# Kernel tuning notes

Hardware: AMD Instinct MI355X
Metric: run time of the kernel (lower is better)

Reference implementation:

```python
import jax, jax.numpy as jnp
import numpy as np

B, IN_DIM, C, H, W = 4, 64, 128, 64, 64
HW = H * W
EPS = 1e-5


def _conv(x, w, b, pad):
    y = jax.lax.conv_general_dilated(
        x, w, (1, 1), [(pad, pad), (pad, pad)],
        dimension_numbers=('NCHW', 'OIHW', 'NCHW'))
    return y + b[None, :, None, None]


def _ln_chw(x, g, b):
    # torch LayerNorm([C,H,W]): normalize over (C,H,W) per sample, affine per-element
    m = jnp.mean(x, axis=(1, 2, 3), keepdims=True)
    v = jnp.mean((x - m) ** 2, axis=(1, 2, 3), keepdims=True)
    return (x - m) * jax.lax.rsqrt(v + EPS) * g[None] + b[None]


def _lrelu(x):
    return jnp.where(x >= 0, x, 0.01 * x)


def setup_inputs():
    ks = jax.random.split(jax.random.key(0), 16)

    def n(i, shape, s):
        return jax.random.normal(ks[i], shape, jnp.float32) * s

    inp = {
        'f_e': n(0, (B, IN_DIM, H, W), 1.0),
        'f_i': n(1, (B, IN_DIM, H, W), 1.0),
        'w1': n(2, (C, IN_DIM, 3, 3), 0.04), 'b1': jnp.zeros((C,), jnp.float32),
        'g1': jnp.ones((C, H, W), jnp.float32), 'be1': jnp.zeros((C, H, W), jnp.float32),
        'w2': n(3, (C, IN_DIM, 3, 3), 0.04), 'b2': jnp.zeros((C,), jnp.float32),
        'g2': jnp.ones((C, H, W), jnp.float32), 'be2': jnp.zeros((C, H, W), jnp.float32),
        'W3': n(4, (HW, HW), 0.015), 'b3': jnp.zeros((HW,), jnp.float32),
        'W4': n(5, (C, C), 0.08), 'b4': jnp.zeros((C,), jnp.float32),
        'W5': n(6, (C, C), 0.08), 'b5': jnp.zeros((C,), jnp.float32),
        'w6a': n(7, (C, C, 1, 1), 0.08), 'b6a': jnp.zeros((C,), jnp.float32),
        'g6a': jnp.ones((C, H, W), jnp.float32), 'be6a': jnp.zeros((C, H, W), jnp.float32),
        'w6b': n(8, (C, C, 3, 3), 0.03), 'b6b': jnp.zeros((C,), jnp.float32),
        'g6b': jnp.ones((C, H, W), jnp.float32), 'be6b': jnp.zeros((C, H, W), jnp.float32),
        'wf': n(9, (IN_DIM, C, 1, 1), 0.08), 'bf': jnp.zeros((IN_DIM,), jnp.float32),
    }
    return inp


def reference(f_e, f_i, w1, b1, g1, be1, w2, b2, g2, be2, W3, b3, W4, b4,
              W5, b5, w6a, b6a, g6a, be6a, w6b, b6b, g6b, be6b, wf, bf):
    b_, _, h, w = f_e.shape
    c = w1.shape[0]
    hw = h * w

    # f_1: conv3x3 -> LN([C,H,W]) -> LeakyReLU -> b (hw) c
    x1 = _lrelu(_ln_chw(_conv(f_e, w1, b1, 1), g1, be1))
    f_e_1 = x1.transpose(0, 2, 3, 1).reshape(b_, hw, c)

    # f_2: conv3x3 -> LN -> LeakyReLU (stays b c h w)
    f_i_2 = _lrelu(_ln_chw(_conv(f_i, w2, b2, 1), g2, be2))

    # f_3: b c (hw) -> Linear(HW,HW) -> LeakyReLU
    f_i_3 = _lrelu(jnp.einsum('bcn,mn->bcm', f_i_2.reshape(b_, c, hw), W3) + b3)

    # f_4: b (hw) c -> Linear(C,C) -> LeakyReLU
    tok = f_i_2.transpose(0, 2, 3, 1).reshape(b_, hw, c)
    f_e_4 = _lrelu(jnp.einsum('bnc,dc->bnd', tok, W4) + b4)

    # unscaled single-head attention over hw tokens
    scores = jnp.einsum('bnc,bcm->bnm', f_e_4, f_i_3)   # (b, hw, hw)
    attn = jax.nn.softmax(scores, axis=-1)
    f_e_5_in = jnp.einsum('bnm,bmc->bnc', attn, f_e_1)

    # f_5: Linear(C,C) -> LeakyReLU -> b c h w
    f_e_5 = _lrelu(jnp.einsum('bnc,dc->bnd', f_e_5_in, W5) + b5)
    f_e_5 = f_e_5.reshape(b_, h, w, c).transpose(0, 3, 1, 2)

    # f_6: conv1x1 -> LN -> LReLU -> conv3x3 -> LN -> LReLU
    y = _lrelu(_ln_chw(_conv(f_i_2, w6a, b6a, 0), g6a, be6a))
    f_i_6 = _lrelu(_ln_chw(_conv(y, w6b, b6b, 1), g6b, be6b))

    f_e_7 = f_e_5 * f_i_6
    f_e_8 = _conv(f_e_7, wf, bf, 0)
    return (f_e_8, f_i_2)
```

## Files before the change

### kernel.cpp

```cpp
#include <hip/hip_runtime.h>

typedef unsigned short ushort_t;
typedef unsigned int uint_t;
typedef unsigned long long u64_t;

#define Bn 4
#define IND 64
#define Cn 128
#define Nn 4096
#define CN 524288
#define BUF 2097152

typedef __attribute__((ext_vector_type(8))) __bf16 bf16x8;
typedef __attribute__((ext_vector_type(4))) float f32x4;

__device__ __forceinline__ float b2f(ushort_t s) {
    return __uint_as_float(((uint_t)s) << 16);
}
__device__ __forceinline__ ushort_t f2b(float f) {
    uint_t u = __float_as_uint(f);
    uint_t r = u + 0x7fffu + ((u >> 16) & 1u);
    return (ushort_t)(r >> 16);
}
__device__ __forceinline__ void unpack8(uint4 u, float* f) {
    f[0] = __uint_as_float(u.x << 16); f[1] = __uint_as_float(u.x & 0xffff0000u);
    f[2] = __uint_as_float(u.y << 16); f[3] = __uint_as_float(u.y & 0xffff0000u);
    f[4] = __uint_as_float(u.z << 16); f[5] = __uint_as_float(u.z & 0xffff0000u);
    f[6] = __uint_as_float(u.w << 16); f[7] = __uint_as_float(u.w & 0xffff0000u);
}
__device__ __forceinline__ float lrelu(float x) { return x >= 0.f ? x : 0.01f * x; }

__device__ __forceinline__ float getv(const float* p, size_t i) { return p[i]; }
__device__ __forceinline__ float getv(const ushort_t* p, size_t i) { return b2f(p[i]); }
__device__ __forceinline__ float4 get4(const float* p, size_t i) { return *(const float4*)(p + i); }
__device__ __forceinline__ float4 get4(const ushort_t* p, size_t i) {
    ushort4 u = *(const ushort4*)(p + i);
    float4 f = {b2f(u.x), b2f(u.y), b2f(u.z), b2f(u.w)};
    return f;
}
__device__ __forceinline__ void stv(float* p, float v) { *p = v; }
__device__ __forceinline__ void stv(ushort_t* p, float v) { *p = f2b(v); }

__device__ __forceinline__ uint4 pack8(float4 a, float4 b) {
    uint4 r;
    r.x = (uint_t)f2b(a.x) | ((uint_t)f2b(a.y) << 16);
    r.y = (uint_t)f2b(a.z) | ((uint_t)f2b(a.w) << 16);
    r.z = (uint_t)f2b(b.x) | ((uint_t)f2b(b.y) << 16);
    r.w = (uint_t)f2b(b.z) | ((uint_t)f2b(b.w) << 16);
    return r;
}

__global__ void detect_kernel(const void* g1, int* flag) {
    if (threadIdx.x == 0 && blockIdx.x == 0)
        *flag = (((const ushort_t*)g1)[0] == 0x3F80) ? 0 : 1;
}

template <int CI>
__global__ __launch_bounds__(256) void wtrans(const void* w, ushort_t* Wt, const int* flagp) {
    int F = *flagp;
    int idx = blockIdx.x * 256 + threadIdx.x;
    if (idx >= 128 * 9 * CI) return;
    int co = idx / (9 * CI);
    int rem = idx - co * 9 * CI;
    int tap = rem / CI;
    int ci = rem - tap * CI;
    size_t srci = (size_t)co * CI * 9 + (size_t)ci * 9 + tap;
    float v = F ? ((const float*)w)[srci] : b2f(((const ushort_t*)w)[srci]);
    Wt[idx] = f2b(v);
}

template <typename TEXT>
__device__ __forceinline__ void tin_body(const TEXT* src, ushort_t* dst, float (*tile)[33]) {
    int b = blockIdx.z, c0 = blockIdx.y * 32, n0 = blockIdx.x * 32;
    int nx = threadIdx.x & 31, cy = threadIdx.x >> 5;
    #pragma unroll
    for (int s = 0; s < 4; s++) {
        int cl = cy + s * 8;
        tile[cl][nx] = getv(src, ((size_t)(b * 64 + c0 + cl)) * 4096 + n0 + nx);
    }
    __syncthreads();
    #pragma unroll
    for (int s = 0; s < 4; s++) {
        int nl = cy + s * 8;
        dst[((size_t)b * 4096 + n0 + nl) * 64 + c0 + nx] = f2b(tile[nx][nl]);
    }
}

__global__ __launch_bounds__(256) void transpose_in(const void* src, ushort_t* dst, const int* flagp) {
    __shared__ float tile[32][33];
    int F = *flagp;
    if (F) tin_body((const float*)src, dst, tile);
    else   tin_body((const ushort_t*)src, dst, tile);
}

template <int CI>
__global__ __launch_bounds__(512, 2) void conv_mfma(const ushort_t* __restrict__ Xt,
                                                    const ushort_t* __restrict__ Wt,
                                                    const void* bias, float* __restrict__ out,
                                                    const int* flagp) {
    constexpr int RS = CI + 8;
    constexpr int SROWS = 195;
    constexpr int SBYTES = SROWS * RS * 2;
    constexpr int OBYTES = 128 * 68 * 4;
    constexpr int SMEM = SBYTES > OBYTES ? SBYTES : OBYTES;
    __shared__ __align__(16) char smem[SMEM];
    ushort_t* S = (ushort_t*)smem;
    float* Ob = (float*)smem;

    int t = threadIdx.x;
    int blk = blockIdx.x;
    int b = blk >> 6, y = blk & 63;
    int n0 = y << 6;

    constexpr int RQ = CI / 8;
    constexpr int CNT = SROWS * RQ;
    for (int i = t; i < CNT; i += 512) {
        int s = i / RQ;
        int c8 = (i - s * RQ) * 8;
        int tok = n0 + s - 65;
        uint4 v = {0u, 0u, 0u, 0u};
        if (s < 194 && (unsigned)tok < 4096u)
            v = *(const uint4*)(Xt + ((size_t)b * 4096 + tok) * CI + c8);
        *(uint4*)(S + (size_t)s * RS + c8) = v;
    }
    __syncthreads();

    int lane = t & 63, w = t >> 6;
    int li = lane & 15, q = lane >> 4;
    int px0 = 16 * (w & 3);
    int coh = 64 * (w >> 2);
    int x = px0 + li;

    f32x4 acc[4];
    #pragma unroll
    for (int T = 0; T < 4; T++) acc[T] = {0.f, 0.f, 0.f, 0.f};

    #pragma unroll
    for (int tap = 0; tap < 9; tap++) {
        int dy = tap / 3 - 1, dx = tap % 3 - 1;
        bool vx = (unsigned)(x + dx) < 64u;
        int srow = x + dy * 64 + dx + 65;
        int sr2 = vx ? srow : 194;
        #pragma unroll
        for (int ks = 0; ks < CI / 32; ks++) {
            bf16x8 a = *(const bf16x8*)(S + (size_t)sr2 * RS + ks * 32 + q * 8);
            #pragma unroll
            for (int T = 0; T < 4; T++) {
                int co = coh + 16 * T + li;
                bf16x8 bb = *(const bf16x8*)(Wt + ((size_t)co * 9 + tap) * CI + ks * 32 + q * 8);
                acc[T] = __builtin_amdgcn_mfma_f32_16x16x32_bf16(a, bb, acc[T], 0, 0, 0);
            }
        }
    }
    __syncthreads();

    int F = *flagp;
    #pragma unroll
    for (int T = 0; T < 4; T++) {
        int co = coh + 16 * T + li;
        float bv = F ? ((const float*)bias)[co] : b2f(((const ushort_t*)bias)[co]);
        #pragma unroll
        for (int rr = 0; rr < 4; rr++)
            Ob[(size_t)co * 68 + px0 + 4 * q + rr] = acc[T][rr] + bv;
    }
    __syncthreads();
    for (int i = t; i < 2048; i += 512) {
        int co = i >> 4, p4 = (i & 15) * 4;
        *(uint4*)(out + ((size_t)(b * 128 + co)) * 4096 + n0 + p4) =
            *(const uint4*)(Ob + (size_t)co * 68 + p4);
    }
}

__global__ __launch_bounds__(256) void ln_reduce1(const float* __restrict__ src,
                                                  float* __restrict__ part) {
    int t = threadIdx.x;
    size_t base = (size_t)blockIdx.x * 1024 + t * 4;
    float4 v = *(const float4*)(src + base);
    float s = v.x + v.y + v.z + v.w;
    float q = v.x * v.x + v.y * v.y + v.z * v.z + v.w * v.w;
    for (int off = 32; off > 0; off >>= 1) {
        s += __shfl_down(s, off, 64);
        q += __shfl_down(q, off, 64);
    }
    __shared__ float red[8];
    if ((t & 63) == 0) { red[(t >> 6) * 2] = s; red[(t >> 6) * 2 + 1] = q; }
    __syncthreads();
    if (t == 0) {
        s = red[0] + red[2] + red[4] + red[6];
        q = red[1] + red[3] + red[5] + red[7];
        part[blockIdx.x * 2] = s;
        part[blockIdx.x * 2 + 1] = q;
    }
}

__global__ __launch_bounds__(256) void ln_reduce2(const float* __restrict__ part,
                                                  float* __restrict__ der) {
    int b = blockIdx.x, t = threadIdx.x;
    float s = part[(b * 512 + t) * 2] + part[(b * 512 + 256 + t) * 2];
    float q = part[(b * 512 + t) * 2 + 1] + part[(b * 512 + 256 + t) * 2 + 1];
    for (int off = 32; off > 0; off >>= 1) {
        s += __shfl_down(s, off, 64);
        q += __shfl_down(q, off, 64);
    }
    __shared__ float red[8];
    if ((t & 63) == 0) { red[(t >> 6) * 2] = s; red[(t >> 6) * 2 + 1] = q; }
    __syncthreads();
    if (t == 0) {
        s = red[0] + red[2] + red[4] + red[6];
        q = red[1] + red[3] + red[5] + red[7];
        float mean = s * (1.f / (float)CN);
        float var = q * (1.f / (float)CN) - mean * mean;
        der[b * 2] = mean;
        der[b * 2 + 1] = rsqrtf(var + 1e-5f);
    }
}

template <typename TEXT, typename TOD, int HT, int HD>
__device__ __forceinline__ void ln_body(const float* src, const TEXT* g, const TEXT* be,
                                        const float* der, ushort_t* outT, TOD* outD,
                                        float (*tile)[33]) {
    int b = blockIdx.z, c0 = blockIdx.y * 32, n0 = blockIdx.x * 32;
    float mean = der[b * 2], rstd = der[b * 2 + 1];
    int nx = threadIdx.x & 31, cy = threadIdx.x >> 5;
    #pragma unroll
    for (int s = 0; s < 4; s++) {
        int cl = cy + s * 8;
        int c = c0 + cl;
        size_t gi = (size_t)c * Nn + n0 + nx;
        float v = (src[(size_t)b * CN + gi] - mean) * rstd * getv(g, gi) + getv(be, gi);
        v = lrelu(v);
        if (HD) stv(outD + (size_t)b * CN + gi, v);
        tile[cl][nx] = v;
    }
    if (HT) {
        __syncthreads();
        #pragma unroll
        for (int s = 0; s < 4; s++) {
            int nl = cy + s * 8;
            int n = n0 + nl;
            int c = c0 + nx;
            outT[((size_t)b * Nn + n) * Cn + c] = f2b(tile[nx][nl]);
        }
    }
}

template <int HT, int HD, int DEXT>
__global__ __launch_bounds__(256) void ln_apply(const float* src, const void* g, const void* be,
                                                const float* der, ushort_t* outT, void* outD,
                                                long doff, const int* flagp) {
    __shared__ float tile[32][33];
    int F = *flagp;
    if (F) {
        if (DEXT && HD)
            ln_body<float, float, HT, HD>(src, (const float*)g, (const float*)be, der, outT,
                                          ((float*)outD) + doff, tile);
        else
            ln_body<float, ushort_t, HT, HD>(src, (const float*)g, (const float*)be, der, outT,
                                             ((ushort_t*)outD) + doff, tile);
    } else {
        ln_body<ushort_t, ushort_t, HT, HD>(src, (const ushort_t*)g, (const ushort_t*)be, der, outT,
                                            ((ushort_t*)outD) + doff, tile);
    }
}

template <int ACT, int TRANS, typename TA, typename TW, typename TO>
__device__ __forceinline__ void gemm_body(const TA* A, const TW* W, const TW* bias, TO* out,
                                          int M, int K, int Rper,
                                          float (*As)[68], float (*Bs)[68]) {
    int m0 = blockIdx.x << 6, r0 = blockIdx.y << 6;
    int t = threadIdx.x, tx = t & 15, ty = t >> 4;
    int sr = t >> 2, sk = (t & 3) << 2;
    float acc[4][4] = {{0.f}};
    for (int kt = 0; kt < K; kt += 16) {
        float4 av = get4(A, (size_t)(r0 + sr) * K + kt + sk);
        float4 wv = get4(W, (size_t)(m0 + sr) * K + kt + sk);
        As[sk + 0][sr] = av.x; As[sk + 1][sr] = av.y;
        As[sk + 2][sr] = av.z; As[sk + 3][sr] = av.w;
        Bs[sk + 0][sr] = wv.x; Bs[sk + 1][sr] = wv.y;
        Bs[sk + 2][sr] = wv.z; Bs[sk + 3][sr] = wv.w;
        __syncthreads();
        #pragma unroll
        for (int kk = 0; kk < 16; kk++) {
            float4 a4 = *(const float4*)&As[kk][ty << 2];
            float4 b4 = *(const float4*)&Bs[kk][tx << 2];
            float aa[4] = {a4.x, a4.y, a4.z, a4.w};
            float bb[4] = {b4.x, b4.y, b4.z, b4.w};
            #pragma unroll
            for (int ii = 0; ii < 4; ii++)
                #pragma unroll
                for (int jj = 0; jj < 4; jj++)
                    acc[ii][jj] += aa[ii] * bb[jj];
        }
        __syncthreads();
    }
    float bv[4];
    #pragma unroll
    for (int jj = 0; jj < 4; jj++) bv[jj] = getv(bias, m0 + (tx << 2) + jj);
    #pragma unroll
    for (int ii = 0; ii < 4; ii++) {
        int r = r0 + (ty << 2) + ii;
        float v[4];
        #pragma unroll
        for (int jj = 0; jj < 4; jj++) {
            float x = acc[ii][jj] + bv[jj];
            if (ACT) x = lrelu(x);
            v[jj] = x;
        }
        if (TRANS) {
            int rb = r / Rper, ri = r % Rper;
            #pragma unroll
            for (int jj = 0; jj < 4; jj++) {
                int m = m0 + (tx << 2) + jj;
                stv(out + ((size_t)rb * M + m) * Rper + ri, v[jj]);
            }
        } else {
            #pragma unroll
            for (int jj = 0; jj < 4; jj++)
                stv(out + (size_t)r * M + m0 + (tx << 2) + jj, v[jj]);
        }
    }
}

template <int ACT, int TRANS, int AK, typename TO>
__global__ __launch_bounds__(256) void gemm_nt(const void* A, long aoff, const void* W,
                                               const void* bias, TO* out, int M, int K, int Rper,
                                               const int* flagp) {
    __shared__ float As[16][68];
    __shared__ float Bs[16][68];
    int F = *flagp;
    if (AK == 0) {
        if (F) gemm_body<ACT, TRANS>((const ushort_t*)A + aoff, (const float*)W, (const float*)bias, out, M, K, Rper, As, Bs);
        else   gemm_body<ACT, TRANS>((const ushort_t*)A + aoff, (const ushort_t*)W, (const ushort_t*)bias, out, M, K, Rper, As, Bs);
    } else if (AK == 1) {
        if (F) gemm_body<ACT, TRANS>((const float*)A + aoff, (const float*)W, (const float*)bias, out, M, K, Rper, As, Bs);
        else   gemm_body<ACT, TRANS>((const float*)A + aoff, (const ushort_t*)W, (const ushort_t*)bias, out, M, K, Rper, As, Bs);
    } else {
        if (F) gemm_body<ACT, TRANS>((const float*)A + aoff, (const float*)W, (const float*)bias, out, M, K, Rper, As, Bs);
        else   gemm_body<ACT, TRANS>((const ushort_t*)A + aoff, (const ushort_t*)W, (const ushort_t*)bias, out, M, K, Rper, As, Bs);
    }
}

__global__ __launch_bounds__(256) void a_convert(const void* src, long aoff, ushort_t* dst,
                                                 const int* flagp) {
    int F = *flagp;
    int gid = blockIdx.x * 256 + threadIdx.x;
    int r = gid >> 9;
    int n0 = (gid & 511) << 3;
    size_t doff = ((size_t)(n0 >> 6) << 15) + ((size_t)r << 6) + (n0 & 63);
    if (F) {
        const float* s = (const float*)src + aoff + (size_t)r * 4096 + n0;
        *(uint4*)(dst + doff) = pack8(*(const float4*)s, *(const float4*)(s + 4));
    } else {
        const ushort_t* s = (const ushort_t*)src + aoff + (size_t)r * 4096 + n0;
        *(uint4*)(dst + doff) = *(const uint4*)s;
    }
}

__global__ __launch_bounds__(256, 2) void gemm_big4(const ushort_t* __restrict__ Ap,
                                                    const void* __restrict__ W3,
                                                    float* __restrict__ C0,
                                                    float* __restrict__ C1,
                                                    const int* flagp) {
    __shared__ __align__(16) char smem[36864];
    ushort_t* Als = (ushort_t*)smem;
    ushort_t* Bls = (ushort_t*)(smem + 18432);
    float* Ot = (float*)smem;

    int F = *flagp;
    int t = threadIdx.x;
    int m0 = blockIdx.x << 6;
    int rb = blockIdx.y;
    int ksl = blockIdx.z;
    int kbase = ksl << 11;

    int lane = t & 63, w = t >> 6;
    int li = lane & 15, q = lane >> 4;
    int wr = w & 1, wc = w >> 1;

    const ushort_t* Asrc = Ap + (((size_t)ksl * 32) << 15) + ((size_t)rb << 13) + t * 8;
    const float* Wf = (const float*)W3;
    const ushort_t* Wh = (const ushort_t*)W3;
    int brow4 = t >> 4, bcol4 = (t & 15) * 4;
    int brow8 = t >> 3, bcol8 = (t & 7) * 8;
    int arow = t >> 3;

    f32x4 acc[4][2];
    #pragma unroll
    for (int i = 0; i < 4; i++)
        #pragma unroll
        for (int j = 0; j < 2; j++) acc[i][j] = {0.f, 0.f, 0.f, 0.f};

    {
        #pragma unroll
        for (int i = 0; i < 4; i++) {
            uint4 v = *(const uint4*)(Asrc + i * 2048);
            *(uint4*)(Als + (size_t)(i * 32 + arow) * 72 + bcol8) = v;
        }
        if (F) {
            #pragma unroll
            for (int i = 0; i < 4; i++) {
                int row = i * 16 + brow4;
                float4 wv = *(const float4*)(Wf + (size_t)(m0 + row) * 4096 + kbase + bcol4);
                ushort4 u = {f2b(wv.x), f2b(wv.y), f2b(wv.z), f2b(wv.w)};
                *(ushort4*)(Bls + (size_t)row * 72 + bcol4) = u;
            }
        } else {
            #pragma unroll
            for (int i = 0; i < 2; i++) {
                int row = i * 32 + brow8;
                uint4 v = *(const uint4*)(Wh + (size_t)(m0 + row) * 4096 + kbase + bcol8);
                *(uint4*)(Bls + (size_t)row * 72 + bcol8) = v;
            }
        }
    }
    __syncthreads();

    for (int kt = 0; kt < 2048; kt += 64) {
        uint4 pa[4];
        float4 pbf[4];
        uint4 pbu[2];
        bool pf = kt < 1984;
        if (pf) {
            const ushort_t* As2 = Asrc + ((size_t)(kt + 64) << 9);
            #pragma unroll
            for (int i = 0; i < 4; i++) pa[i] = *(const uint4*)(As2 + i * 2048);
            if (F) {
                #pragma unroll
                for (int i = 0; i < 4; i++) {
                    int row = i * 16 + brow4;
                    pbf[i] = *(const float4*)(Wf + (size_t)(m0 + row) * 4096 + kbase + kt + 64 + bcol4);
                }
            } else {
                #pragma unroll
                for (int i = 0; i < 2; i++) {
                    int row = i * 32 + brow8;
                    pbu[i] = *(const uint4*)(Wh + (size_t)(m0 + row) * 4096 + kbase + kt + 64 + bcol8);
                }
            }
        }
        __builtin_amdgcn_s_setprio(1);
        #pragma unroll
        for (int ks = 0; ks < 2; ks++) {
            bf16x8 af[4], bfr[2];
            #pragma unroll
            for (int rf = 0; rf < 4; rf++)
                af[rf] = *(const bf16x8*)(Als + (size_t)(64 * wr + 16 * rf + li) * 72 + ks * 32 + q * 8);
            #pragma unroll
            for (int cf = 0; cf < 2; cf++)
                bfr[cf] = *(const bf16x8*)(Bls + (size_t)(32 * wc + 16 * cf + li) * 72 + ks * 32 + q * 8);
            #pragma unroll
            for (int rf = 0; rf < 4; rf++)
                #pragma unroll
                for (int cf = 0; cf < 2; cf++)
                    acc[rf][cf] = __builtin_amdgcn_mfma_f32_16x16x32_bf16(af[rf], bfr[cf], acc[rf][cf], 0, 0, 0);
        }
        __builtin_amdgcn_s_setprio(0);
        __syncthreads();
        if (pf) {
            #pragma unroll
            for (int i = 0; i < 4; i++)
                *(uint4*)(Als + (size_t)(i * 32 + arow) * 72 + bcol8) = pa[i];
            if (F) {
                #pragma unroll
                for (int i = 0; i < 4; i++) {
                    int row = i * 16 + brow4;
                    ushort4 u = {f2b(pbf[i].x), f2b(pbf[i].y), f2b(pbf[i].z), f2b(pbf[i].w)};
                    *(ushort4*)(Bls + (size_t)row * 72 + bcol4) = u;
                }
            } else {
                #pragma unroll
                for (int i = 0; i < 2; i++)
                    *(uint4*)(Bls + (size_t)(i * 32 + brow8) * 72 + bcol8) = pbu[i];
            }
            __syncthreads();
        }
    }

    #pragma unroll
    for (int rf = 0; rf < 4; rf++)
        #pragma unroll
        for (int cf = 0; cf < 2; cf++)
            #pragma unroll
            for (int rr = 0; rr < 4; rr++)
                Ot[(size_t)(64 * wr + 16 * rf + 4 * q + rr) * 72 + 32 * wc + 16 * cf + li] = acc[rf][cf][rr];
    __syncthreads();
    float* Pc = (ksl == 0 ? C0 : C1) + (size_t)(rb * 128) * 4096;
    for (int g = t; g < 2048; g += 256) {
        int row = g >> 4, c4 = (g & 15) * 4;
        *(float4*)(Pc + (size_t)row * 4096 + m0 + c4) = *(const float4*)(Ot + (size_t)row * 72 + c4);
    }
}

__global__ __launch_bounds__(256) void gemm_merge(const float* __restrict__ C0,
                                                  const float* __restrict__ C1,
                                                  const void* b3, ushort_t* __restrict__ out,
                                                  const int* flagp) {
    __shared__ float tile[32][33];
    int F = *flagp;
    int m0 = blockIdx.x * 32, c0 = blockIdx.y * 32, b = blockIdx.z;
    int nx = threadIdx.x & 31, cy = threadIdx.x >> 5;
    float bv = F ? ((const float*)b3)[m0 + nx] : b2f(((const ushort_t*)b3)[m0 + nx]);
    #pragma unroll
    for (int s = 0; s < 4; s++) {
        int cl = cy + s * 8;
        size_t ri = (size_t)(b * 128 + c0 + cl) * 4096 + m0 + nx;
        tile[cl][nx] = lrelu(C0[ri] + C1[ri] + bv);
    }
    __syncthreads();
    #pragma unroll
    for (int s = 0; s < 4; s++) {
        int ml = cy + s * 8;
        out[((size_t)b * 4096 + m0 + ml) * 128 + c0 + nx] = f2b(tile[nx][ml]);
    }
}

__global__ __launch_bounds__(256, 2) void attn_mfma(const ushort_t* __restrict__ Q,
                                                    const ushort_t* __restrict__ Kg,
                                                    const ushort_t* __restrict__ Vg,
                                                    ushort_t* __restrict__ Op0,
                                                    ushort_t* __restrict__ Op1,
                                                    ushort_t* __restrict__ Op2,
                                                    ushort_t* __restrict__ Op3,
                                                    float* __restrict__ ML) {
    __shared__ __align__(16) ushort_t Ks[64 * 136];
    __shared__ __align__(16) ushort_t Vt[128 * 72];
    __shared__ __align__(16) ushort_t Ps[128 * 88];

    int t = threadIdx.x;
    int blk = blockIdx.x;
    int h = blk >> 7;
    int rblk = blk & 127;
    int b = rblk & 3;
    int qt = rblk >> 2;
    int n0 = qt << 7;
    int lane = t & 63, w = t >> 6;
    int li = lane & 15, q = lane >> 4;

    int kj = t >> 2, kc0 = (t & 3) * 32;
    int vd = t >> 1, vk0 = (t & 1) * 32;

    int kt0 = h << 4;
    int m00 = kt0 << 6;

    {
        const ushort_t* kp = Kg + ((size_t)(b * Nn + m00 + kj)) * 128 + kc0;
        ushort_t* dst = Ks + kj * 136 + kc0;
        #pragma unroll
        for (int cc = 0; cc < 4; cc++)
            *(uint4*)(dst + cc * 8) = *(const uint4*)(kp + cc * 8);
    }
    {
        const ushort_t* vp = Vg + (size_t)b * CN + (size_t)vd * Nn + m00 + vk0;
        ushort_t* dst = Vt + vd * 72 + vk0;
        #pragma unroll
        for (int cc = 0; cc < 4; cc++)
            *(uint4*)(dst + cc * 8) = *(const uint4*)(vp + cc * 8);
    }

    bf16x8 qf[2][4];
    #pragma unroll
    for (int sub = 0; sub < 2; sub++)
        #pragma unroll
        for (int ks = 0; ks < 4; ks++)
            qf[sub][ks] = *(const bf16x8*)(Q +
                ((size_t)(b * Nn + n0 + 32 * w + 16 * sub + li)) * 128 + ks * 32 + q * 8);

    f32x4 acc[2][8];
    #pragma unroll
    for (int sub = 0; sub < 2; sub++)
        #pragma unroll
        for (int T = 0; T < 8; T++) acc[sub][T] = {0.f, 0.f, 0.f, 0.f};
    float m_i[2][4], l_i[2][4];
    #pragma unroll
    for (int sub = 0; sub < 2; sub++)
        #pragma unroll
        for (int r = 0; r < 4; r++) { m_i[sub][r] = -1e30f; l_i[sub][r] = 0.f; }

    __syncthreads();

    for (int kt = kt0; kt < kt0 + 16; kt++) {
        uint4 pk[4], pv[4];
        bool pf = kt < kt0 + 15;
        if (pf) {
            int m1 = (kt + 1) << 6;
            const ushort_t* kp = Kg + ((size_t)(b * Nn + m1 + kj)) * 128 + kc0;
            #pragma unroll
            for (int cc = 0; cc < 4; cc++) pk[cc] = *(const uint4*)(kp + cc * 8);
            const ushort_t* vp = Vg + (size_t)b * CN + (size_t)vd * Nn + m1 + vk0;
            #pragma unroll
            for (int cc = 0; cc < 4; cc++) pv[cc] = *(const uint4*)(vp + cc * 8);
        }

        f32x4 s[2][4];
        #pragma unroll
        for (int sub = 0; sub < 2; sub++)
            #pragma unroll
            for (int T = 0; T < 4; T++) s[sub][T] = {0.f, 0.f, 0.f, 0.f};
        __builtin_amdgcn_s_setprio(1);
        #pragma unroll
        for (int ks = 0; ks < 4; ks++) {
            bf16x8 a0 = qf[0][ks];
            bf16x8 a1 = qf[1][ks];
            #pragma unroll
            for (int T = 0; T < 4; T++) {
                bf16x8 kb = *(const bf16x8*)(Ks + (16 * T + li) * 136 + ks * 32 + q * 8);
                s[0][T] = __builtin_amdgcn_mfma_f32_16x16x32_bf16(a0, kb, s[0][T], 0, 0, 0);
                s[1][T] = __builtin_amdgcn_mfma_f32_16x16x32_bf16(a1, kb, s[1][T], 0, 0, 0);
            }
        }
        __builtin_amdgcn_s_setprio(0);

        float rm[2][4];
        bool grow = false;
        #pragma unroll
        for (int sub = 0; sub < 2; sub++)
            #pragma unroll
            for (int r = 0; r < 4; r++) {
                float v = fmaxf(fmaxf(s[sub][0][r], s[sub][1][r]),
                                fmaxf(s[sub][2][r], s[sub][3][r]));
                v = fmaxf(v, __shfl_xor(v, 1, 64));
                v = fmaxf(v, __shfl_xor(v, 2, 64));
                v = fmaxf(v, __shfl_xor(v, 4, 64));
                v = fmaxf(v, __shfl_xor(v, 8, 64));
                rm[sub][r] = v;
                grow = grow || (v > m_i[sub][r]);
            }
        if (__any(grow)) {
            #pragma unroll
            for (int sub = 0; sub < 2; sub++)
                #pragma unroll
                for (int r = 0; r < 4; r++) {
                    float mnew = fmaxf(m_i[sub][r], rm[sub][r]);
                    float al = __expf(m_i[sub][r] - mnew);
                    m_i[sub][r] = mnew;
                    float rsum = 0.f;
                    #pragma unroll
                    for (int T = 0; T < 4; T++) {
                        float pvv = __expf(s[sub][T][r] - mnew);
                        Ps[(32 * w + 16 * sub + 4 * q + r) * 88 + 16 * T + li] = f2b(pvv);
                        rsum += pvv;
                    }
                    l_i[sub][r] = l_i[sub][r] * al + rsum;
                    #pragma unroll
                    for (int T = 0; T < 8; T++) acc[sub][T][r] *= al;
                }
        } else {
            #pragma unroll
            for (int sub = 0; sub < 2; sub++)
                #pragma unroll
                for (int r = 0; r < 4; r++) {
                    float rsum = 0.f;
                    #pragma unroll
                    for (int T = 0; T < 4; T++) {
                        float pvv = __expf(s[sub][T][r] - m_i[sub][r]);
                        Ps[(32 * w + 16 * sub + 4 * q + r) * 88 + 16 * T + li] = f2b(pvv);
                        rsum += pvv;
                    }
                    l_i[sub][r] += rsum;
                }
        }

        __builtin_amdgcn_s_setprio(1);
        #pragma unroll
        for (int ks = 0; ks < 2; ks++) {
            bf16x8 pa0 = *(const bf16x8*)(Ps + (32 * w + li) * 88 + ks * 32 + q * 8);
            bf16x8 pa1 = *(const bf16x8*)(Ps + (32 * w + 16 + li) * 88 + ks * 32 + q * 8);
            #pragma unroll
            for (int T = 0; T < 8; T++) {
                bf16x8 vb = *(const bf16x8*)(Vt + (16 * T + li) * 72 + ks * 32 + q * 8);
                acc[0][T] = __builtin_amdgcn_mfma_f32_16x16x32_bf16(pa0, vb, acc[0][T], 0, 0, 0);
                acc[1][T] = __builtin_amdgcn_mfma_f32_16x16x32_bf16(pa1, vb, acc[1][T], 0, 0, 0);
            }
        }
        __builtin_amdgcn_s_setprio(0);
        __syncthreads();
        if (pf) {
            ushort_t* dk = Ks + kj * 136 + kc0;
            #pragma unroll
            for (int cc = 0; cc < 4; cc++) *(uint4*)(dk + cc * 8) = pk[cc];
            ushort_t* dv = Vt + vd * 72 + vk0;
            #pragma unroll
            for (int cc = 0; cc < 4; cc++) *(uint4*)(dv + cc * 8) = pv[cc];
            __syncthreads();
        }
    }

    #pragma unroll
    for (int sub = 0; sub < 2; sub++)
        #pragma unroll
        for (int r = 0; r < 4; r++) {
            float ls = l_i[sub][r];
            ls += __shfl_xor(ls, 1, 64);
            ls += __shfl_xor(ls, 2, 64);
            ls += __shfl_xor(ls, 4, 64);
            ls += __shfl_xor(ls, 8, 64);
            l_i[sub][r] = ls;
        }

    ushort_t* Op = (h == 0) ? Op0 : (h == 1) ? Op1 : (h == 2) ? Op2 : Op3;
    #pragma unroll
    for (int sub = 0; sub < 2; sub++)
        #pragma unroll
        for (int T = 0; T < 8; T++)
            #pragma unroll
            for (int r = 0; r < 4; r++) {
                int n = n0 + 32 * w + 16 * sub + 4 * q + r;
                int d = 16 * T + li;
                Op[((size_t)(b * Nn + n)) * 128 + d] = f2b(acc[sub][T][r]);
            }
    if (li == 0) {
        #pragma unroll
        for (int sub = 0; sub < 2; sub++)
            #pragma unroll
            for (int r = 0; r < 4; r++) {
                int n = n0 + 32 * w + 16 * sub + 4 * q + r;
                size_t mi = ((size_t)(h * Bn + b) * Nn + n) * 2;
                ML[mi] = m_i[sub][r];
                ML[mi + 1] = l_i[sub][r];
            }
    }
}

__global__ __launch_bounds__(256) void attn_merge(const ushort_t* __restrict__ Op0,
                                                  const ushort_t* __restrict__ Op1,
                                                  const ushort_t* __restrict__ Op2,
                                                  const ushort_t* __restrict__ Op3,
                                                  const float* __restrict__ ML,
                                                  float* __restrict__ Og) {
    int idx = blockIdx.x * 256 + threadIdx.x;
    int token = idx >> 4;
    int c8 = (idx & 15) * 8;
    float m[4], l[4];
    #pragma unroll
    for (int s = 0; s < 4; s++) {
        m[s] = ML[((size_t)s * (Bn * Nn) + token) * 2];
        l[s] = ML[((size_t)s * (Bn * Nn) + token) * 2 + 1];
    }
    float M = fmaxf(fmaxf(m[0], m[1]), fmaxf(m[2], m[3]));
    float e[4];
    float denom = 0.f;
    #pragma unroll
    for (int s = 0; s < 4; s++) { e[s] = __expf(m[s] - M); denom += l[s] * e[s]; }
    float inv = 1.f / denom;
    #pragma unroll
    for (int s = 0; s < 4; s++) e[s] *= inv;
    uint4 u0 = *(const uint4*)(Op0 + (size_t)token * 128 + c8);
    uint4 u1 = *(const uint4*)(Op1 + (size_t)token * 128 + c8);
    uint4 u2 = *(const uint4*)(Op2 + (size_t)token * 128 + c8);
    uint4 u3 = *(const uint4*)(Op3 + (size_t)token * 128 + c8);
    float f0[8], f1[8], f2[8], f3[8];
    unpack8(u0, f0);
    unpack8(u1, f1);
    unpack8(u2, f2);
    unpack8(u3, f3);
    float o[8];
    #pragma unroll
    for (int j = 0; j < 8; j++)
        o[j] = f0[j] * e[0] + f1[j] * e[1] + f2[j] * e[2] + f3[j] * e[3];
    float4 v0 = {o[0], o[1], o[2], o[3]};
    float4 v1 = {o[4], o[5], o[6], o[7]};
    float* op = Og + (size_t)token * 128 + c8;
    *(float4*)op = v0;
    *(float4*)(op + 4) = v1;
}

template <typename TEXT, typename TOUT>
__device__ __forceinline__ void final_body(const ushort_t* fe5, const ushort_t* fi6t,
                                           const TEXT* wf, const TEXT* bf, TOUT* out0,
                                           float* prod, ushort_t* wfs, float* bfs) {
    int t = threadIdx.x;
    int b = blockIdx.x >> 6;
    int px0 = (blockIdx.x & 63) * 64;
    for (int idx = t * 4; idx < 8192; idx += 1024) {
        float4 v = get4(wf, idx);
        ushort4 u = {f2b(v.x), f2b(v.y), f2b(v.z), f2b(v.w)};
        *(ushort4*)&wfs[idx] = u;
    }
    if (t < 64) bfs[t] = getv(bf, t);
    {
        int pix = t >> 2, kc = (t & 3) * 32;
        const ushort_t* ap = fe5 + ((size_t)(b * Nn + px0 + pix)) * 128 + kc;
        const ushort_t* bp = fi6t + ((size_t)(b * Nn + px0 + pix)) * 128 + kc;
        #pragma unroll
        for (int c = 0; c < 4; c++) {
            uint4 ua = *(const uint4*)(ap + c * 8);
            uint4 ub = *(const uint4*)(bp + c * 8);
            float fa[8], fb[8];
            unpack8(ua, fa);
            unpack8(ub, fb);
            float* pp = &prod[pix * 132 + kc + c * 8];
            #pragma unroll
            for (int j = 0; j < 8; j++) pp[j] = fa[j] * fb[j];
        }
    }
    __syncthreads();
    int pix = t >> 2, og = t & 3;
    for (int k = 0; k < 16; k++) {
        int o = og * 16 + k;
        float a = bfs[o];
        for (int kc = 0; kc < 128; kc += 8) {
            uint4 wu = *(const uint4*)&wfs[o * 128 + kc];
            float w8[8];
            unpack8(wu, w8);
            const float* pp = &prod[pix * 132 + kc];
            float4 p0 = *(const float4*)pp;
            float4 p1 = *(const float4*)(pp + 4);
            a += w8[0] * p0.x + w8[1] * p0.y + w8[2] * p0.z + w8[3] * p0.w
               + w8[4] * p1.x + w8[5] * p1.y + w8[6] * p1.z + w8[7] * p1.w;
        }
        stv(out0 + ((size_t)(b * 64 + o)) * Nn + px0 + pix, a);
    }
}

__global__ __launch_bounds__(256) void final_out(const ushort_t* fe5, const ushort_t* fi6t,
                                                 const void* wf, const void* bf, void* out0,
                                                 const int* flagp) {
    __shared__ __align__(16) float prod[64 * 132];
    __shared__ __align__(16) ushort_t wfs[64 * 128];
    __shared__ float bfs[64];
    int F = *flagp;
    if (F) final_body((const ushort_t*)fe5, fi6t, (const float*)wf, (const float*)bf, (float*)out0, prod, wfs, bfs);
    else   final_body((const ushort_t*)fe5, fi6t, (const ushort_t*)wf, (const ushort_t*)bf, (ushort_t*)out0, prod, wfs, bfs);
}

extern "C" void kernel_launch(void* const* d_in, const int* in_sizes, int n_in,
                              void* d_out, int out_size, void* d_ws, size_t ws_size,
                              hipStream_t stream) {
    const void* f_e = d_in[0];
    const void* f_i = d_in[1];
    const void* w1 = d_in[2];
    const void* b1 = d_in[3];
    const void* g1 = d_in[4];
    const void* be1 = d_in[5];
    const void* w2 = d_in[6];
    const void* b2 = d_in[7];
    const void* g2 = d_in[8];
    const void* be2 = d_in[9];
    const void* W3 = d_in[10];
    const void* b3 = d_in[11];
    const void* W4 = d_in[12];
    const void* b4 = d_in[13];
    const void* W5 = d_in[14];
    const void* b5 = d_in[15];
    const void* w6a = d_in[16];
    const void* b6a = d_in[17];
    const void* g6a = d_in[18];
    const void* be6a = d_in[19];
    const void* w6b = d_in[20];
    const void* b6b = d_in[21];
    const void* g6b = d_in[22];
    const void* be6b = d_in[23];
    const void* wf = d_in[24];
    const void* bf = d_in[25];

    char* wsb = (char*)d_ws;
    int* FLAG = (int*)wsb;
    float* PART = (float*)(wsb + 1024);
    float* DER  = (float*)(wsb + 17408);
    ushort_t* Wt1  = (ushort_t*)(wsb + 32768);
    ushort_t* Wt2  = (ushort_t*)(wsb + 180224);
    ushort_t* Wt6b = (ushort_t*)(wsb + 327680);
    float* ML   = (float*)(wsb + 32768);
    float* TMP  = (float*)(wsb + 622592);
    ushort_t* FE1  = (ushort_t*)(wsb + 9011200);
    ushort_t* TOK  = FE1 + BUF;
    ushort_t* FI3T = TOK + BUF;
    ushort_t* FE4  = FI3T + BUF;
    ushort_t* Y6   = FE4 + BUF;
    ushort_t* FI6T = Y6 + BUF;

    ushort_t* FEt = FI3T;
    ushort_t* FIt = FE4;

    float* C0 = TMP;
    float* C1 = (float*)FE4;
    ushort_t* ABF = FI6T;

    ushort_t* OPA = (ushort_t*)TMP;
    ushort_t* OPB = OPA + BUF;
    float* MRG = (float*)FI3T;

    const long OUT1OFF = (long)Bn * IND * Nn;

    dim3 lnGrid(128, 4, 4);
    dim3 tinGrid(128, 2, 4);

    detect_kernel<<<1, 64, 0, stream>>>(g1, FLAG);

    wtrans<64><<<288, 256, 0, stream>>>(w1, Wt1, FLAG);
    wtrans<64><<<288, 256, 0, stream>>>(w2, Wt2, FLAG);
    wtrans<128><<<576, 256, 0, stream>>>(w6b, Wt6b, FLAG);

    transpose_in<<<tinGrid, 256, 0, stream>>>(f_e, FEt, FLAG);
    conv_mfma<64><<<256, 512, 0, stream>>>(FEt, Wt1, b1, TMP, FLAG);
    ln_reduce1<<<2048, 256, 0, stream>>>(TMP, PART);
    ln_reduce2<<<4, 256, 0, stream>>>(PART, DER);
    ln_apply<0, 1, 0><<<lnGrid, 256, 0, stream>>>(TMP, g1, be1, DER, nullptr, FE1, 0, FLAG);

    transpose_in<<<tinGrid, 256, 0, stream>>>(f_i, FIt, FLAG);
    conv_mfma<64><<<256, 512, 0, stream>>>(FIt, Wt2, b2, TMP, FLAG);
    ln_reduce1<<<2048, 256, 0, stream>>>(TMP, PART);
    ln_reduce2<<<4, 256, 0, stream>>>(PART, DER);
    ln_apply<1, 1, 1><<<lnGrid, 256, 0, stream>>>(TMP, g2, be2, DER, TOK, d_out, OUT1OFF, FLAG);

    a_convert<<<1024, 256, 0, stream>>>(d_out, OUT1OFF, ABF, FLAG);
    gemm_big4<<<dim3(64, 4, 2), 256, 0, stream>>>(ABF, W3, C0, C1, FLAG);
    gemm_merge<<<dim3(128, 4, 4), 256, 0, stream>>>(C0, C1, b3, FI3T, FLAG);

    gemm_nt<1, 0, 0, ushort_t><<<dim3(2, 256), 256, 0, stream>>>(TOK, 0, W4, b4, FE4, 128, 128, 1, FLAG);

    gemm_nt<0, 1, 0, float><<<dim3(2, 256), 256, 0, stream>>>(TOK, 0, w6a, b6a, TMP, 128, 128, 4096, FLAG);
    ln_reduce1<<<2048, 256, 0, stream>>>(TMP, PART);
    ln_reduce2<<<4, 256, 0, stream>>>(PART, DER);
    ln_apply<1, 0, 0><<<lnGrid, 256, 0, stream>>>(TMP, g6a, be6a, DER, Y6, nullptr, 0, FLAG);

    conv_mfma<128><<<256, 512, 0, stream>>>(Y6, Wt6b, b6b, TMP, FLAG);
    ln_reduce1<<<2048, 256, 0, stream>>>(TMP, PART);
    ln_reduce2<<<4, 256, 0, stream>>>(PART, DER);
    ln_apply<1, 0, 0><<<lnGrid, 256, 0, stream>>>(TMP, g6b, be6b, DER, FI6T, nullptr, 0, FLAG);

    attn_mfma<<<512, 256, 0, stream>>>(FE4, FI3T, FE1, TOK, Y6, OPA, OPB, ML);
    attn_merge<<<1024, 256, 0, stream>>>(TOK, Y6, OPA, OPB, ML, MRG);

    gemm_nt<1, 0, 1, ushort_t><<<dim3(2, 256), 256, 0, stream>>>(MRG, 0, W5, b5, Y6, 128, 128, 1, FLAG);

    final_out<<<256, 256, 0, stream>>>(Y6, FI6T, wf, bf, d_out, FLAG);
}
```

Baseline: 554.0 us.

## Rewrite W3 GEMM with direct global-to-LDS loads, XOR swizzle, 4-way split-K

Replaces the big HW×HW GEMM kernel with one that stages A and W3 tiles straight into LDS with global_load_lds on an XOR-swizzled layout, which a_convert now writes to match. This removes the register round-trip and the padded-stride staging. Split-K grows from 2 to 4 slices and occupancy is raised to 4 blocks per CU, giving more parallelism. Partial results are stored as bf16 instead of fp32 to cut write traffic, at some accuracy cost when the merge kernel sums four partials. In fp32 mode W3 is now staged as fp32 in LDS and converted at fragment load, and the loop runs unpipelined (load, then sync, then compute).

Measured after the change: 521.7 us. -5.8%, faster.

```diff
diff --git a/kernel.cpp b/kernel.cpp
--- a/kernel.cpp
+++ b/kernel.cpp
@@ -346,7 +346,8 @@
     int gid = blockIdx.x * 256 + threadIdx.x;
     int r = gid >> 9;
     int n0 = (gid & 511) << 3;
-    size_t doff = ((size_t)(n0 >> 6) << 15) + ((size_t)r << 6) + (n0 & 63);
+    int gs = ((n0 >> 3) & 7) ^ (r & 7);
+    size_t doff = ((size_t)(n0 >> 6) << 15) + ((size_t)r << 6) + ((size_t)gs << 3);
     if (F) {
         const float* s = (const float*)src + aoff + (size_t)r * 4096 + n0;
         *(uint4*)(dst + doff) = pack8(*(const float4*)s, *(const float4*)(s + 4));
@@ -356,33 +357,23 @@
     }
 }
 
-__global__ __launch_bounds__(256, 2) void gemm_big4(const ushort_t* __restrict__ Ap,
-                                                    const void* __restrict__ W3,
-                                                    float* __restrict__ C0,
-                                                    float* __restrict__ C1,
-                                                    const int* flagp) {
-    __shared__ __align__(16) char smem[36864];
-    ushort_t* Als = (ushort_t*)smem;
-    ushort_t* Bls = (ushort_t*)(smem + 18432);
-    float* Ot = (float*)smem;
-
-    int F = *flagp;
+template <int F>
+__device__ __forceinline__ void gemm6_body(const ushort_t* __restrict__ Ap,
+                                           const void* __restrict__ W3,
+                                           ushort_t* __restrict__ Pc,
+                                           char* smem) {
     int t = threadIdx.x;
     int m0 = blockIdx.x << 6;
     int rb = blockIdx.y;
     int ksl = blockIdx.z;
-    int kbase = ksl << 11;
-
     int lane = t & 63, w = t >> 6;
     int li = lane & 15, q = lane >> 4;
     int wr = w & 1, wc = w >> 1;
-
-    const ushort_t* Asrc = Ap + (((size_t)ksl * 32) << 15) + ((size_t)rb << 13) + t * 8;
-    const float* Wf = (const float*)W3;
-    const ushort_t* Wh = (const ushort_t*)W3;
-    int brow4 = t >> 4, bcol4 = (t & 15) * 4;
-    int brow8 = t >> 3, bcol8 = (t & 7) * 8;
-    int arow = t >> 3;
+    int kbase = ksl << 10;
+
+    const char* Ab = (const char*)Ap;
+    const char* Wb = (const char*)W3;
+    size_t Abase = ((size_t)(ksl * 16) << 16) + ((size_t)rb << 14);
 
     f32x4 acc[4][2];
     #pragma unroll
@@ -390,109 +381,133 @@
         #pragma unroll
         for (int j = 0; j < 2; j++) acc[i][j] = {0.f, 0.f, 0.f, 0.f};
 
-    {
+    auto stageA = [&](int kt64) {
+        size_t tb = Abase + ((size_t)kt64 << 16);
         #pragma unroll
         for (int i = 0; i < 4; i++) {
-            uint4 v = *(const uint4*)(Asrc + i * 2048);
-            *(uint4*)(Als + (size_t)(i * 32 + arow) * 72 + bcol8) = v;
-        }
+            int loff = w * 4096 + i * 1024;
+            __builtin_amdgcn_global_load_lds(
+                (const uint_t*)(Ab + tb + loff + lane * 16),
+                (uint_t*)(smem + loff), 16, 0, 0);
+        }
+    };
+    auto stageB = [&](int kt) {
         if (F) {
             #pragma unroll
             for (int i = 0; i < 4; i++) {
-                int row = i * 16 + brow4;
-                float4 wv = *(const float4*)(Wf + (size_t)(m0 + row) * 4096 + kbase + bcol4);
-                ushort4 u = {f2b(wv.x), f2b(wv.y), f2b(wv.z), f2b(wv.w)};
-                *(ushort4*)(Bls + (size_t)row * 72 + bcol4) = u;
+                int loff = w * 4096 + i * 1024;
+                int L = loff + lane * 16;
+                int row = L >> 8, inner = L & 255;
+                int sg = (inner >> 5) ^ (row & 7);
+                __builtin_amdgcn_global_load_lds(
+                    (const uint_t*)(Wb + ((size_t)(m0 + row) << 14) +
+                                    (size_t)(kbase + kt) * 4 + (sg << 5) + (inner & 31)),
+                    (uint_t*)(smem + 16384 + loff), 16, 0, 0);
             }
         } else {
             #pragma unroll
             for (int i = 0; i < 2; i++) {
-                int row = i * 32 + brow8;
-                uint4 v = *(const uint4*)(Wh + (size_t)(m0 + row) * 4096 + kbase + bcol8);
-                *(uint4*)(Bls + (size_t)row * 72 + bcol8) = v;
-            }
-        }
-    }
-    __syncthreads();
-
-    for (int kt = 0; kt < 2048; kt += 64) {
-        uint4 pa[4];
-        float4 pbf[4];
-        uint4 pbu[2];
-        bool pf = kt < 1984;
-        if (pf) {
-            const ushort_t* As2 = Asrc + ((size_t)(kt + 64) << 9);
-            #pragma unroll
-            for (int i = 0; i < 4; i++) pa[i] = *(const uint4*)(As2 + i * 2048);
+                int loff = w * 2048 + i * 1024;
+                int L = loff + lane * 16;
+                int row = L >> 7, inner = L & 127;
+                int sg = (inner >> 4) ^ (row & 7);
+                __builtin_amdgcn_global_load_lds(
+                    (const uint_t*)(Wb + ((size_t)(m0 + row) << 13) +
+                                    (size_t)(kbase + kt) * 2 + (sg << 4)),
+                    (uint_t*)(smem + 16384 + loff), 16, 0, 0);
+            }
+        }
+    };
+
+    stageA(0);
+    stageB(0);
+    for (int it = 0; it < 16; it++) {
+        __syncthreads();
+        const ushort_t* As = (const ushort_t*)smem;
+        #pragma unroll
+        for (int ks = 0; ks < 2; ks++) {
+            int gsw = ks * 4 + q;
+            int sw = (gsw ^ (li & 7)) << 3;
+            bf16x8 af[4], bfr[2];
+            #pragma unroll
+            for (int rf = 0; rf < 4; rf++) {
+                int row = 64 * wr + 16 * rf + li;
+                af[rf] = *(const bf16x8*)(As + row * 64 + sw);
+            }
             if (F) {
+                const float* Bf = (const float*)(smem + 16384);
                 #pragma unroll
-                for (int i = 0; i < 4; i++) {
-                    int row = i * 16 + brow4;
-                    pbf[i] = *(const float4*)(Wf + (size_t)(m0 + row) * 4096 + kbase + kt + 64 + bcol4);
+                for (int cf = 0; cf < 2; cf++) {
+                    int row = 32 * wc + 16 * cf + li;
+                    const float* p = Bf + row * 64 + sw;
+                    float4 lo = *(const float4*)p;
+                    float4 hi = *(const float4*)(p + 4);
+                    bf16x8 v;
+                    v[0] = (__bf16)lo.x; v[1] = (__bf16)lo.y;
+                    v[2] = (__bf16)lo.z; v[3] = (__bf16)lo.w;
+                    v[4] = (__bf16)hi.x; v[5] = (__bf16)hi.y;
+                    v[6] = (__bf16)hi.z; v[7] = (__bf16)hi.w;
+                    bfr[cf] = v;
                 }
             } else {
+                const ushort_t* Bs = (const ushort_t*)(smem + 16384);
                 #pragma unroll
-                for (int i = 0; i < 2; i++) {
-                    int row = i * 32 + brow8;
-                    pbu[i] = *(const uint4*)(Wh + (size_t)(m0 + row) * 4096 + kbase + kt + 64 + bcol8);
+                for (int cf = 0; cf < 2; cf++) {
+                    int row = 32 * wc + 16 * cf + li;
+                    bfr[cf] = *(const bf16x8*)(Bs + row * 64 + sw);
                 }
             }
-        }
-        __builtin_amdgcn_s_setprio(1);
-        #pragma unroll
-        for (int ks = 0; ks < 2; ks++) {
-            bf16x8 af[4], bfr[2];
-            #pragma unroll
-            for (int rf = 0; rf < 4; rf++)
-                af[rf] = *(const bf16x8*)(Als + (size_t)(64 * wr + 16 * rf + li) * 72 + ks * 32 + q * 8);
-            #pragma unroll
-            for (int cf = 0; cf < 2; cf++)
-                bfr[cf] = *(const bf16x8*)(Bls + (size_t)(32 * wc + 16 * cf + li) * 72 + ks * 32 + q * 8);
             #pragma unroll
             for (int rf = 0; rf < 4; rf++)
                 #pragma unroll
                 for (int cf = 0; cf < 2; cf++)
                     acc[rf][cf] = __builtin_amdgcn_mfma_f32_16x16x32_bf16(af[rf], bfr[cf], acc[rf][cf], 0, 0, 0);
         }
-        __builtin_amdgcn_s_setprio(0);
         __syncthreads();
-        if (pf) {
-            #pragma unroll
-            for (int i = 0; i < 4; i++)
-                *(uint4*)(Als + (size_t)(i * 32 + arow) * 72 + bcol8) = pa[i];
-            if (F) {
-                #pragma unroll
-                for (int i = 0; i < 4; i++) {
-                    int row = i * 16 + brow4;
-                    ushort4 u = {f2b(pbf[i].x), f2b(pbf[i].y), f2b(pbf[i].z), f2b(pbf[i].w)};
-                    *(ushort4*)(Bls + (size_t)row * 72 + bcol4) = u;
-                }
-            } else {
-                #pragma unroll
-                for (int i = 0; i < 2; i++)
-                    *(uint4*)(Bls + (size_t)(i * 32 + brow8) * 72 + bcol8) = pbu[i];
-            }
-            __syncthreads();
-        }
-    }
-
+        if (it < 15) {
+            stageA(it + 1);
+            stageB((it + 1) << 6);
+        }
+    }
+
+    ushort_t* Ot = (ushort_t*)smem;
     #pragma unroll
     for (int rf = 0; rf < 4; rf++)
         #pragma unroll
         for (int cf = 0; cf < 2; cf++)
             #pragma unroll
             for (int rr = 0; rr < 4; rr++)
-                Ot[(size_t)(64 * wr + 16 * rf + 4 * q + rr) * 72 + 32 * wc + 16 * cf + li] = acc[rf][cf][rr];
+                Ot[(64 * wr + 16 * rf + 4 * q + rr) * 72 + 32 * wc + 16 * cf + li] =
+                    f2b(acc[rf][cf][rr]);
     __syncthreads();
-    float* Pc = (ksl == 0 ? C0 : C1) + (size_t)(rb * 128) * 4096;
-    for (int g = t; g < 2048; g += 256) {
-        int row = g >> 4, c4 = (g & 15) * 4;
-        *(float4*)(Pc + (size_t)row * 4096 + m0 + c4) = *(const float4*)(Ot + (size_t)row * 72 + c4);
-    }
-}
-
-__global__ __launch_bounds__(256) void gemm_merge(const float* __restrict__ C0,
-                                                  const float* __restrict__ C1,
+    #pragma unroll
+    for (int i = 0; i < 4; i++) {
+        int idx = t + i * 256;
+        int row = idx >> 3, c8 = (idx & 7) * 8;
+        *(uint4*)(Pc + ((size_t)(rb * 128 + row)) * 4096 + m0 + c8) =
+            *(const uint4*)(Ot + row * 72 + c8);
+    }
+}
+
+__global__ __launch_bounds__(256, 4) void gemm_big6(const ushort_t* __restrict__ Ap,
+                                                    const void* __restrict__ W3,
+                                                    ushort_t* __restrict__ C0,
+                                                    ushort_t* __restrict__ C1,
+                                                    ushort_t* __restrict__ C2,
+                                                    ushort_t* __restrict__ C3,
+                                                    const int* flagp) {
+    __shared__ __align__(16) char smem[32768];
+    int F = *flagp;
+    int ksl = blockIdx.z;
+    ushort_t* Pc = (ksl == 0) ? C0 : (ksl == 1) ? C1 : (ksl == 2) ? C2 : C3;
+    if (F) gemm6_body<1>(Ap, W3, Pc, smem);
+    else   gemm6_body<0>(Ap, W3, Pc, smem);
+}
+
+__global__ __launch_bounds__(256) void gemm_merge(const ushort_t* __restrict__ C0,
+                                                  const ushort_t* __restrict__ C1,
+                                                  const ushort_t* __restrict__ C2,
+                                                  const ushort_t* __restrict__ C3,
                                                   const void* b3, ushort_t* __restrict__ out,
                                                   const int* flagp) {
     __shared__ float tile[32][33];
@@ -504,7 +519,7 @@
     for (int s = 0; s < 4; s++) {
         int cl = cy + s * 8;
         size_t ri = (size_t)(b * 128 + c0 + cl) * 4096 + m0 + nx;
-        tile[cl][nx] = lrelu(C0[ri] + C1[ri] + bv);
+        tile[cl][nx] = lrelu(b2f(C0[ri]) + b2f(C1[ri]) + b2f(C2[ri]) + b2f(C3[ri]) + bv);
     }
     __syncthreads();
     #pragma unroll
@@ -872,8 +887,10 @@
     ushort_t* FEt = FI3T;
     ushort_t* FIt = FE4;
 
-    float* C0 = TMP;
-    float* C1 = (float*)FE4;
+    ushort_t* C0b = (ushort_t*)TMP;
+    ushort_t* C1b = C0b + BUF;
+    ushort_t* C2b = FE4;
+    ushort_t* C3b = Y6;
     ushort_t* ABF = FI6T;
 
     ushort_t* OPA = (ushort_t*)TMP;
@@ -904,8 +921,8 @@
     ln_apply<1, 1, 1><<<lnGrid, 256, 0, stream>>>(TMP, g2, be2, DER, TOK, d_out, OUT1OFF, FLAG);
 
     a_convert<<<1024, 256, 0, stream>>>(d_out, OUT1OFF, ABF, FLAG);
-    gemm_big4<<<dim3(64, 4, 2), 256, 0, stream>>>(ABF, W3, C0, C1, FLAG);
-    gemm_merge<<<dim3(128, 4, 4), 256, 0, stream>>>(C0, C1, b3, FI3T, FLAG);
+    gemm_big6<<<dim3(64, 4, 4), 256, 0, stream>>>(ABF, W3, C0b, C1b, C2b, C3b, FLAG);
+    gemm_merge<<<dim3(128, 4, 4), 256, 0, stream>>>(C0b, C1b, C2b, C3b, b3, FI3T, FLAG);
 
     gemm_nt<1, 0, 0, ushort_t><<<dim3(2, 256), 256, 0, stream>>>(TOK, 0, W4, b4, FE4, 128, 128, 1, FLAG);
 
```
